# Optimization experiments

Measured on AMD Instinct MI355X. Metric: run time of the kernel, lower is better.

Reference implementation:

```python
import jax, jax.numpy as jnp
import numpy as np

R = 21
STRIDE = 2
ETA = 0.01
H = W = 147
HP = WP = 64
PI = np.pi
TAU = 0.1


def _unfold(img):
    # img: (N, C, H, W) -> patches (N, C, R, R, HP, WP), patch[h,w] starts at (h*STRIDE, w*STRIDE)
    hidx = jnp.arange(HP) * STRIDE          # (HP,)
    widx = jnp.arange(WP) * STRIDE          # (WP,)
    ridx = jnp.arange(R)
    rows = hidx[:, None] + ridx[None, :]    # (HP, R)
    cols = widx[:, None] + ridx[None, :]    # (WP, R)
    p = img[:, :, rows, :]                  # (N, C, HP, R, W)
    p = p[:, :, :, :, cols]                 # (N, C, HP, R, WP, R)
    return jnp.transpose(p, (0, 1, 3, 5, 2, 4))  # (N, C, R, R, HP, WP)


def _params2dists(params, x, y, tau=TAU):
    # params: (N, 5, HP, WP); x, y: (1, R, R, 1, 1)
    x0 = params[:, 3][:, None, None]        # (N,1,1,HP,WP)
    y0 = params[:, 4][:, None, None]
    ang = jnp.sort(jnp.mod(params[:, :3], 2 * PI), axis=1)
    a1 = ang[:, 0][:, None, None]
    a2 = ang[:, 1][:, None, None]
    a3 = ang[:, 2][:, None, None]
    a4 = 0.5 * (a1 + a3) + jnp.where(jnp.mod(0.5 * (a1 - a3), 2 * PI) >= PI, PI, 0.0)

    def g(dtheta):
        return (dtheta / PI - 1.0) ** 35

    def line(a):
        # signed distance to line through (x0,y0) at angle a: (N, R, R, HP, WP)
        return -jnp.sin(a) * (x - x0) + jnp.cos(a) * (y - y0)

    sgn42 = jnp.where(jnp.mod(a2 - a4, 2 * PI) < PI, 1.0, -1.0)
    dist42 = sgn42 * jnp.minimum(sgn42 * line(a4), -sgn42 * line(a2)) + g(jnp.mod(a2 - a4, 2 * PI)) * tau
    sgn13 = jnp.where(jnp.mod(a3 - a1, 2 * PI) < PI, 1.0, -1.0)
    dist13 = sgn13 * jnp.minimum(sgn13 * line(a1), -sgn13 * line(a3)) + g(jnp.mod(a3 - a1, 2 * PI)) * tau
    return jnp.stack([dist13, dist42], axis=1)  # (N, 2, R, R, HP, WP)


def _dists2indicators(dists):
    h = 0.5 * (1.0 + (2.0 / PI) * jnp.arctan(dists / ETA))
    return jnp.stack([1.0 - h[:, 0],
                      h[:, 0] * (1.0 - h[:, 1]),
                      h[:, 0] * h[:, 1]], axis=1)  # (N, 3, R, R, HP, WP)


def setup_inputs() -> dict:
    key = jax.random.key(0)
    k1, k2, k3 = jax.random.split(key, 3)
    ests = jax.random.normal(k1, (1, HP * WP, 5), dtype=jnp.float32)
    noisy_image = jax.random.uniform(k2, (1, H, W, 3), dtype=jnp.float32)
    gt_image = jax.random.uniform(k3, (1, H, W, 3), dtype=jnp.float32)
    return {"ests": ests, "noisy_image": noisy_image, "gt_image": gt_image, "alpha": 1}


def reference(ests, noisy_image, gt_image, alpha):
    # colors_only=True path of Assistance.forward
    grid = jnp.linspace(-1.0, 1.0, R)
    yv, xv = jnp.meshgrid(grid, grid, indexing="ij")
    x = xv.reshape(1, R, R, 1, 1)
    y = yv.reshape(1, R, R, 1, 1)

    e = jnp.transpose(ests, (0, 2, 1)).reshape(1, 5, HP, WP)
    angles = jnp.sort(jnp.mod((e[:, :3] + 1.0) * PI, 2 * PI), axis=1)
    x0y0 = e[:, 3:] * 3.0
    para = jnp.concatenate([angles, x0y0], axis=1)   # (1, 5, HP, WP)

    img_patches = _unfold(jnp.transpose(noisy_image, (0, 3, 1, 2)))  # (1,3,R,R,HP,WP)

    dists = _params2dists(para, x, y)
    wedges = _dists2indicators(dists)                # (1,3,R,R,HP,WP)
    # numerator: sum over patch pixels of img * wedge indicator
    num = jnp.einsum("ncrshw,nkrshw->nckhw", img_patches, wedges)
    wsum = wedges.sum(axis=(2, 3))                   # (1,3,HP,WP)
    colors = num / (wsum[:, None] + 1e-10)           # (1,3,3,HP,WP)
    return colors
```

## Files before the change

### kernel.cpp

```cpp
#include <hip/hip_runtime.h>
#include <hip/hip_bf16.h>
#include <math.h>

#define RR 21
#define HPX 64
#define WPX 64
#define IMGW 147
#define PI_F 3.14159265358979323846f
#define TWO_PI_F 6.28318530717958647692f
#define TAU_F 0.1f

__device__ __forceinline__ float mod2pi(float x) {
    float r = fmodf(x, TWO_PI_F);
    return r < 0.f ? r + TWO_PI_F : r;
}

__device__ __forceinline__ float gpow35(float dtheta) {
    float t = dtheta * (1.f / PI_F) - 1.f;
    float t2 = t * t;
    float t4 = t2 * t2;
    float t8 = t4 * t4;
    float t16 = t8 * t8;
    float t32 = t16 * t16;
    return t32 * t2 * t;
}

__global__ __launch_bounds__(256) void wedge_colors_kernel(
    const float* __restrict__ ests,
    const float* __restrict__ img,
    float* __restrict__ out)
{
    const int wave = threadIdx.x >> 6;
    const int lane = threadIdx.x & 63;
    const int p = blockIdx.x * 4 + wave;
    const int ph = p >> 6;
    const int pw = p & 63;

    const float* e = ests + p * 5;
    float b0 = mod2pi((e[0] + 1.f) * PI_F);
    float b1 = mod2pi((e[1] + 1.f) * PI_F);
    float b2 = mod2pi((e[2] + 1.f) * PI_F);
    float a1 = fminf(b0, fminf(b1, b2));
    float a3 = fmaxf(b0, fmaxf(b1, b2));
    float a2 = (b0 + b1 + b2) - a1 - a3;
    float x0 = e[3] * 3.f;
    float y0 = e[4] * 3.f;

    float mhalf = mod2pi(0.5f * (a1 - a3));
    float a4 = 0.5f * (a1 + a3) + (mhalf >= PI_F ? PI_F : 0.f);

    float d42 = mod2pi(a2 - a4);
    float d13 = mod2pi(a3 - a1);
    float sgn42 = (d42 < PI_F) ? 1.f : -1.f;
    float sgn13 = (d13 < PI_F) ? 1.f : -1.f;
    float g42 = gpow35(d42) * TAU_F;
    float g13 = gpow35(d13) * TAU_F;

    float s1, c1, s2, c2, s3, c3, s4, c4;
    sincosf(a1, &s1, &c1);
    sincosf(a2, &s2, &c2);
    sincosf(a3, &s3, &c3);
    sincosf(a4, &s4, &c4);

    float acc[12];
#pragma unroll
    for (int i = 0; i < 12; i++) acc[i] = 0.f;

    for (int idx = lane; idx < RR * RR; idx += 64) {
        int r = idx / RR;
        int s = idx - r * RR;
        float x = (float)s * 0.1f - 1.f;
        float y = (float)r * 0.1f - 1.f;
        float dx = x - x0;
        float dy = y - y0;

        float L1 = -s1 * dx + c1 * dy;
        float L2 = -s2 * dx + c2 * dy;
        float L3 = -s3 * dx + c3 * dy;
        float L4 = -s4 * dx + c4 * dy;

        float dist13 = sgn13 * fminf(sgn13 * L1, -sgn13 * L3) + g13;
        float dist42 = sgn42 * fminf(sgn42 * L4, -sgn42 * L2) + g42;

        float h0 = 0.5f + 0.318309886183790672f * atanf(dist13 * 100.f);
        float h1 = 0.5f + 0.318309886183790672f * atanf(dist42 * 100.f);

        float w0 = 1.f - h0;
        float w2 = h0 * h1;
        float w1 = h0 - w2;

        const float* px = img + ((ph * 2 + r) * IMGW + (pw * 2 + s)) * 3;
        float p0 = px[0];
        float p1 = px[1];
        float p2 = px[2];

        acc[0] += p0 * w0;  acc[1] += p0 * w1;  acc[2] += p0 * w2;
        acc[3] += p1 * w0;  acc[4] += p1 * w1;  acc[5] += p1 * w2;
        acc[6] += p2 * w0;  acc[7] += p2 * w1;  acc[8] += p2 * w2;
        acc[9] += w0;       acc[10] += w1;      acc[11] += w2;
    }

#pragma unroll
    for (int off = 32; off > 0; off >>= 1) {
#pragma unroll
        for (int i = 0; i < 12; i++) acc[i] += __shfl_xor(acc[i], off, 64);
    }

    if (lane == 0) {
        float inv0 = 1.f / (acc[9]  + 1e-10f);
        float inv1 = 1.f / (acc[10] + 1e-10f);
        float inv2 = 1.f / (acc[11] + 1e-10f);
        const int base = ph * WPX + pw;
        out[0 * 4096 + base] = acc[0] * inv0;
        out[1 * 4096 + base] = acc[1] * inv1;
        out[2 * 4096 + base] = acc[2] * inv2;
        out[3 * 4096 + base] = acc[3] * inv0;
        out[4 * 4096 + base] = acc[4] * inv1;
        out[5 * 4096 + base] = acc[5] * inv2;
        out[6 * 4096 + base] = acc[6] * inv0;
        out[7 * 4096 + base] = acc[7] * inv1;
        out[8 * 4096 + base] = acc[8] * inv2;
    }
}

extern "C" void kernel_launch(void* const* d_in, const int* in_sizes, int n_in,
                              void* d_out, int out_size, void* d_ws, size_t ws_size,
                              hipStream_t stream) {
    const float* ests  = (const float*)d_in[0];
    const float* noisy = (const float*)d_in[1];
    float* out = (float*)d_out;

    wedge_colors_kernel<<<1024, 256, 0, stream>>>(ests, noisy, out);
}
```

Baseline: 68.75 us.

## Restructure wedge loop with fast atan, fixed lane mapping, and algebraic accumulator reduction

Replaces the libm atanf with a minimax polynomial approximation, fmodf with a floor-based mod, and sincosf with fast intrinsics. Remaps the 441 patch pixels onto 63 lanes as 3 rows by 21 columns over 7 unrolled iterations, which removes the per-pixel integer division and hoists the per-column line terms out of the loop. It also folds the sign handling into precomputed coefficients and accumulates only h0 and h0*h1 products, recovering the three wedge sums algebraically, so fewer accumulators are kept and shuffled. The polynomial atan and the fast sin/cos carry accuracy risk near the sharp arctan transition.

```diff
diff --git a/kernel.cpp b/kernel.cpp
--- a/kernel.cpp
+++ b/kernel.cpp
@@ -2,27 +2,41 @@
 #include <hip/hip_bf16.h>
 #include <math.h>
 
-#define RR 21
 #define HPX 64
 #define WPX 64
 #define IMGW 147
 #define PI_F 3.14159265358979323846f
 #define TWO_PI_F 6.28318530717958647692f
+#define INV_TWO_PI_F 0.15915494309189533577f
+#define INV_PI_F 0.31830988618379067154f
 #define TAU_F 0.1f
 
 __device__ __forceinline__ float mod2pi(float x) {
-    float r = fmodf(x, TWO_PI_F);
-    return r < 0.f ? r + TWO_PI_F : r;
+    float t = floorf(x * INV_TWO_PI_F);
+    return fmaf(-t, TWO_PI_F, x);
 }
 
 __device__ __forceinline__ float gpow35(float dtheta) {
-    float t = dtheta * (1.f / PI_F) - 1.f;
+    float t = dtheta * INV_PI_F - 1.f;
     float t2 = t * t;
     float t4 = t2 * t2;
     float t8 = t4 * t4;
     float t16 = t8 * t8;
     float t32 = t16 * t16;
     return t32 * t2 * t;
+}
+
+__device__ __forceinline__ float fast_h(float d) {
+    float z = d * 100.f;
+    float az = fabsf(z);
+    bool big = az > 1.0f;
+    float r = big ? __builtin_amdgcn_rcpf(az) : az;
+    float a = r * r;
+    float pol = r * fmaf(a, fmaf(a, fmaf(a, -0.0851330f, 0.1801410f), -0.3302995f),
+                         0.9998660f);
+    float res = big ? (1.5707963267948966f - pol) : pol;
+    res = copysignf(res, z);
+    return fmaf(res, INV_PI_F, 0.5f);
 }
 
 __global__ __launch_bounds__(256) void wedge_colors_kernel(
@@ -42,84 +56,94 @@
     float b2 = mod2pi((e[2] + 1.f) * PI_F);
     float a1 = fminf(b0, fminf(b1, b2));
     float a3 = fmaxf(b0, fmaxf(b1, b2));
-    float a2 = (b0 + b1 + b2) - a1 - a3;
+    float a2 = fmaxf(fminf(b0, b1), fminf(fmaxf(b0, b1), b2));
     float x0 = e[3] * 3.f;
     float y0 = e[4] * 3.f;
 
     float mhalf = mod2pi(0.5f * (a1 - a3));
     float a4 = 0.5f * (a1 + a3) + (mhalf >= PI_F ? PI_F : 0.f);
 
-    float d42 = mod2pi(a2 - a4);
-    float d13 = mod2pi(a3 - a1);
-    float sgn42 = (d42 < PI_F) ? 1.f : -1.f;
-    float sgn13 = (d13 < PI_F) ? 1.f : -1.f;
-    float g42 = gpow35(d42) * TAU_F;
-    float g13 = gpow35(d13) * TAU_F;
+    float d42m = mod2pi(a2 - a4);
+    float d13m = mod2pi(a3 - a1);
+    float sgn42 = (d42m < PI_F) ? 1.f : -1.f;
+    float sgn13 = (d13m < PI_F) ? 1.f : -1.f;
+    float g42 = gpow35(d42m) * TAU_F;
+    float g13 = gpow35(d13m) * TAU_F;
 
-    float s1, c1, s2, c2, s3, c3, s4, c4;
-    sincosf(a1, &s1, &c1);
-    sincosf(a2, &s2, &c2);
-    sincosf(a3, &s3, &c3);
-    sincosf(a4, &s4, &c4);
+    float s1 = __sinf(a1), c1 = __cosf(a1);
+    float s2 = __sinf(a2), c2 = __cosf(a2);
+    float s3 = __sinf(a3), c3 = __cosf(a3);
+    float s4 = __sinf(a4), c4 = __cosf(a4);
 
-    float acc[12];
+    const int r_off = lane / 21;
+    const int s     = lane - 21 * r_off;
+    float x  = (float)s * 0.1f - 1.f;
+    float dx = x - x0;
+
+    float P1 =  sgn13 * c1, B1 = -sgn13 * s1 * dx;
+    float P3 = -sgn13 * c3, B3 =  sgn13 * s3 * dx;
+    float P4 =  sgn42 * c4, B4 = -sgn42 * s4 * dx;
+    float P2 = -sgn42 * c2, B2 =  sgn42 * s2 * dx;
+
+    float sp0 = 0.f, sp1 = 0.f, sp2 = 0.f;
+    float sa0 = 0.f, sa1 = 0.f, sa2 = 0.f;
+    float sb0 = 0.f, sb1 = 0.f, sb2 = 0.f;
+    float sh = 0.f, su = 0.f;
+
+    if (lane < 63) {
+        const float* base = img + ((2 * ph + r_off) * IMGW + (2 * pw + s)) * 3;
 #pragma unroll
-    for (int i = 0; i < 12; i++) acc[i] = 0.f;
+        for (int k = 0; k < 7; k++) {
+            int r = r_off + 3 * k;
+            float y  = (float)r * 0.1f - 1.f;
+            float dy = y - y0;
 
-    for (int idx = lane; idx < RR * RR; idx += 64) {
-        int r = idx / RR;
-        int s = idx - r * RR;
-        float x = (float)s * 0.1f - 1.f;
-        float y = (float)r * 0.1f - 1.f;
-        float dx = x - x0;
-        float dy = y - y0;
+            const float* px = base + k * (3 * IMGW * 3);
+            float p0 = px[0];
+            float p1 = px[1];
+            float p2 = px[2];
 
-        float L1 = -s1 * dx + c1 * dy;
-        float L2 = -s2 * dx + c2 * dy;
-        float L3 = -s3 * dx + c3 * dy;
-        float L4 = -s4 * dx + c4 * dy;
+            float t1 = fmaf(P1, dy, B1);
+            float t3 = fmaf(P3, dy, B3);
+            float t4 = fmaf(P4, dy, B4);
+            float t2 = fmaf(P2, dy, B2);
 
-        float dist13 = sgn13 * fminf(sgn13 * L1, -sgn13 * L3) + g13;
-        float dist42 = sgn42 * fminf(sgn42 * L4, -sgn42 * L2) + g42;
+            float d13 = fmaf(sgn13, fminf(t1, t3), g13);
+            float d42 = fmaf(sgn42, fminf(t4, t2), g42);
 
-        float h0 = 0.5f + 0.318309886183790672f * atanf(dist13 * 100.f);
-        float h1 = 0.5f + 0.318309886183790672f * atanf(dist42 * 100.f);
+            float h0 = fast_h(d13);
+            float h1 = fast_h(d42);
+            float u  = h0 * h1;
 
-        float w0 = 1.f - h0;
-        float w2 = h0 * h1;
-        float w1 = h0 - w2;
-
-        const float* px = img + ((ph * 2 + r) * IMGW + (pw * 2 + s)) * 3;
-        float p0 = px[0];
-        float p1 = px[1];
-        float p2 = px[2];
-
-        acc[0] += p0 * w0;  acc[1] += p0 * w1;  acc[2] += p0 * w2;
-        acc[3] += p1 * w0;  acc[4] += p1 * w1;  acc[5] += p1 * w2;
-        acc[6] += p2 * w0;  acc[7] += p2 * w1;  acc[8] += p2 * w2;
-        acc[9] += w0;       acc[10] += w1;      acc[11] += w2;
+            sp0 += p0;            sp1 += p1;            sp2 += p2;
+            sa0 = fmaf(p0, h0, sa0); sa1 = fmaf(p1, h0, sa1); sa2 = fmaf(p2, h0, sa2);
+            sb0 = fmaf(p0, u, sb0);  sb1 = fmaf(p1, u, sb1);  sb2 = fmaf(p2, u, sb2);
+            sh += h0;             su += u;
+        }
     }
 
 #pragma unroll
     for (int off = 32; off > 0; off >>= 1) {
-#pragma unroll
-        for (int i = 0; i < 12; i++) acc[i] += __shfl_xor(acc[i], off, 64);
+        sp0 += __shfl_xor(sp0, off, 64); sp1 += __shfl_xor(sp1, off, 64); sp2 += __shfl_xor(sp2, off, 64);
+        sa0 += __shfl_xor(sa0, off, 64); sa1 += __shfl_xor(sa1, off, 64); sa2 += __shfl_xor(sa2, off, 64);
+        sb0 += __shfl_xor(sb0, off, 64); sb1 += __shfl_xor(sb1, off, 64); sb2 += __shfl_xor(sb2, off, 64);
+        sh  += __shfl_xor(sh,  off, 64); su  += __shfl_xor(su,  off, 64);
     }
 
     if (lane == 0) {
-        float inv0 = 1.f / (acc[9]  + 1e-10f);
-        float inv1 = 1.f / (acc[10] + 1e-10f);
-        float inv2 = 1.f / (acc[11] + 1e-10f);
+        float inv0 = 1.f / (441.f - sh + 1e-10f);
+        float inv1 = 1.f / (sh - su + 1e-10f);
+        float inv2 = 1.f / (su + 1e-10f);
         const int base = ph * WPX + pw;
-        out[0 * 4096 + base] = acc[0] * inv0;
-        out[1 * 4096 + base] = acc[1] * inv1;
-        out[2 * 4096 + base] = acc[2] * inv2;
-        out[3 * 4096 + base] = acc[3] * inv0;
-        out[4 * 4096 + base] = acc[4] * inv1;
-        out[5 * 4096 + base] = acc[5] * inv2;
-        out[6 * 4096 + base] = acc[6] * inv0;
-        out[7 * 4096 + base] = acc[7] * inv1;
-        out[8 * 4096 + base] = acc[8] * inv2;
+        out[0 * 4096 + base] = (sp0 - sa0) * inv0;
+        out[1 * 4096 + base] = (sa0 - sb0) * inv1;
+        out[2 * 4096 + base] = sb0 * inv2;
+        out[3 * 4096 + base] = (sp1 - sa1) * inv0;
+        out[4 * 4096 + base] = (sa1 - sb1) * inv1;
+        out[5 * 4096 + base] = sb1 * inv2;
+        out[6 * 4096 + base] = (sp2 - sa2) * inv0;
+        out[7 * 4096 + base] = (sa2 - sb2) * inv1;
+        out[8 * 4096 + base] = sb2 * inv2;
     }
 }
 
```

After: 65.10 us. 5.3% less time.
